# Performance work log

Hardware: AMD Instinct MI355X
Metric: run time of the kernel (lower is better)

Reference implementation:

```python
import jax, jax.numpy as jnp
import numpy as np

B, T, C, H = 4, 2048, 1024, 16
HD = C // H  # head dim = 64


def setup_inputs() -> dict:
    key = jax.random.key(0)
    k1, k2, k3 = jax.random.split(key, 3)
    x = jax.random.normal(k1, (B, T, C), dtype=jnp.float32)
    # nn.Linear weight init scale ~ 1/sqrt(fan_in); keep magnitudes sane
    w_qkv = jax.random.normal(k2, (C, 3 * C), dtype=jnp.float32) * (1.0 / np.sqrt(C))
    w_out = jax.random.normal(k3, (C, C), dtype=jnp.float32) * (1.0 / np.sqrt(C))
    return {"x": x, "w_qkv": w_qkv, "w_out": w_out}


def _attention(x, w_qkv, w_out):
    Bs, Ts, Cs = x.shape
    qkv = x @ w_qkv                                  # [B,T,3C]
    q, k, v = jnp.split(qkv, 3, axis=-1)
    # [B,T,C] -> [B,H,T,hd]
    def heads(t):
        return t.reshape(Bs, Ts, H, HD).transpose(0, 2, 1, 3)
    q, k, v = heads(q), heads(k), heads(v)
    scale = 1.0 / np.sqrt(HD)
    scores = jnp.einsum("bhqd,bhkd->bhqk", q, k) * scale  # [B,H,T,T]
    causal = jnp.tril(jnp.ones((Ts, Ts), dtype=bool))
    scores = jnp.where(causal, scores, jnp.finfo(scores.dtype).min)
    probs = jax.nn.softmax(scores, axis=-1)
    attn = jnp.einsum("bhqk,bhkd->bhqd", probs, v)        # [B,H,T,hd]
    attn = attn.transpose(0, 2, 1, 3).reshape(Bs, Ts, Cs)  # [B,T,C]
    return attn @ w_out  # dropout_p=0 at eval


def reference(x, w_qkv, w_out):
    return _attention(x, w_qkv, w_out)
```

## Files before the change

### kernel.cpp

```cpp
#include <hip/hip_runtime.h>
#include <hip/hip_bf16.h>

#define B_   4
#define T_   2048
#define C_   1024
#define H_   16
#define HD_  64
#define BH_  (B_*H_)
#define M_   (B_*T_)
#define N1_  (3*C_)

typedef __hip_bfloat16 bf16;
typedef __attribute__((ext_vector_type(8))) __bf16 bf16x8v;
typedef __attribute__((ext_vector_type(4))) float  f32x4;

#define QSCALE 0.18033688f

__device__ __forceinline__ f32x4 mfma16(bf16x8v a, bf16x8v b, f32x4 c) {
    return __builtin_amdgcn_mfma_f32_16x16x32_bf16(a, b, c, 0, 0, 0);
}

__device__ __forceinline__ float exp2_hw(float x) {
    return __builtin_amdgcn_exp2f(x);
}

typedef __attribute__((address_space(3))) unsigned int       lds_u32;
typedef const __attribute__((address_space(1))) unsigned int glb_u32;
__device__ __forceinline__ void async16(void* lds, const void* g) {
    __builtin_amdgcn_global_load_lds((glb_u32*)g, (lds_u32*)lds, 16, 0, 0);
}

template<int CTRL>
__device__ __forceinline__ float dpp_rot(float x) {
    int v = __builtin_amdgcn_update_dpp(0, __float_as_int(x), CTRL, 0xF, 0xF, true);
    return __int_as_float(v);
}
__device__ __forceinline__ float row16_sum(float x) {
    x += dpp_rot<0x121>(x);
    x += dpp_rot<0x122>(x);
    x += dpp_rot<0x124>(x);
    x += dpp_rot<0x128>(x);
    return x;
}

__global__ void convert_f32_bf16(const float* __restrict__ in, bf16* __restrict__ out) {
    const int i = blockIdx.x * blockDim.x + threadIdx.x;
    float f[8];
    *(float4*)(f)     = ((const float4*)in)[i*2];
    *(float4*)(f + 4) = ((const float4*)in)[i*2 + 1];
    bf16 t[8];
#pragma unroll
    for (int j = 0; j < 8; ++j) t[j] = __float2bfloat16(f[j]);
    ((uint4*)out)[i] = *(uint4*)t;
}

__global__ void transpose_f32_to_bf16(const float* __restrict__ in,
                                      bf16* __restrict__ out, int K, int N) {
    __shared__ float t[32][33];
    const int n0 = blockIdx.x * 32, k0 = blockIdx.y * 32;
    const int c  = threadIdx.x & 31;
    const int rr = threadIdx.x >> 5;
#pragma unroll
    for (int i = 0; i < 4; ++i)
        t[c][rr + 8*i] = in[(size_t)(k0 + rr + 8*i) * N + n0 + c];
    __syncthreads();
#pragma unroll
    for (int i = 0; i < 4; ++i)
        out[(size_t)(n0 + rr + 8*i) * K + k0 + c] = __float2bfloat16(t[rr + 8*i][c]);
}

template<int EPI>
__global__ __launch_bounds__(256, 2)
void gemm_lds(const bf16* __restrict__ A, const bf16* __restrict__ Bt,
              float* __restrict__ Cmat, int N, int K,
              bf16* __restrict__ qb, bf16* __restrict__ kb, bf16* __restrict__ vb)
{
    __shared__ bf16 Alds[128][32];
    __shared__ bf16 Blds[128][32];

    const int tid  = threadIdx.x;
    const int wave = tid >> 6, lane = tid & 63;
    const int quad = lane >> 4, l16 = lane & 15;
    const int wm   = (wave >> 1) * 64, wn = (wave & 1) * 64;
    const size_t row0 = (size_t)blockIdx.y * 128;
    const size_t col0 = (size_t)blockIdx.x * 128;

    const f32x4 z4 = {0.f, 0.f, 0.f, 0.f};
    f32x4 acc[4][4];
#pragma unroll
    for (int mi = 0; mi < 4; ++mi)
#pragma unroll
        for (int ni = 0; ni < 4; ++ni) acc[mi][ni] = z4;

    const int sr = lane >> 2;
    const int sc = (((lane & 3) ^ ((lane >> 3) & 3))) * 8;
    const bf16* gA0 = A  + (row0 + wave*32 + sr) * (size_t)K + sc;
    const bf16* gA1 = gA0 + (size_t)16 * K;
    const bf16* gB0 = Bt + (col0 + wave*32 + sr) * (size_t)K + sc;
    const bf16* gB1 = gB0 + (size_t)16 * K;
    bf16* lA0 = &Alds[wave*32][0];
    bf16* lA1 = &Alds[wave*32 + 16][0];
    bf16* lB0 = &Blds[wave*32][0];
    bf16* lB1 = &Blds[wave*32 + 16][0];

    const int fg = (quad ^ ((l16 >> 1) & 3)) * 8;

    for (int k0 = 0; k0 < K; k0 += 32) {
        async16(lA0, gA0 + k0);
        async16(lA1, gA1 + k0);
        async16(lB0, gB0 + k0);
        async16(lB1, gB1 + k0);
        __syncthreads();

        bf16x8v af[4], bfr[4];
#pragma unroll
        for (int i = 0; i < 4; ++i) {
            af[i]  = *(const bf16x8v*)(&Alds[wm + i*16 + l16][fg]);
            bfr[i] = *(const bf16x8v*)(&Blds[wn + i*16 + l16][fg]);
        }
#pragma unroll
        for (int mi = 0; mi < 4; ++mi)
#pragma unroll
            for (int ni = 0; ni < 4; ++ni)
                acc[mi][ni] = mfma16(af[mi], bfr[ni], acc[mi][ni]);
        __syncthreads();
    }

#pragma unroll
    for (int mi = 0; mi < 4; ++mi) {
        const size_t rowb = row0 + wm + mi*16 + quad*4;
#pragma unroll
        for (int ni = 0; ni < 4; ++ni) {
            const size_t col = col0 + wn + ni*16 + l16;
#pragma unroll
            for (int r = 0; r < 4; ++r) {
                const float v = acc[mi][ni][r];
                if constexpr (EPI == 0) {
                    Cmat[(rowb + r) * N + col] = v;
                } else {
                    const int rowi = (int)(rowb + r);
                    const int b  = rowi >> 11;
                    const int t  = rowi & (T_ - 1);
                    const int coli = (int)col;
                    const int type = coli >> 10;
                    const int cc2  = coli & (C_ - 1);
                    const int h = cc2 >> 6, d = cc2 & (HD_ - 1);
                    const int bh = b * H_ + h;
                    if (type == 0)
                        qb[((size_t)bh * T_ + t) * HD_ + d] = __float2bfloat16(v * QSCALE);
                    else if (type == 1)
                        kb[((size_t)bh * T_ + t) * HD_ + d] = __float2bfloat16(v);
                    else
                        vb[((size_t)bh * HD_ + d) * T_ + t] = __float2bfloat16(v);
                }
            }
        }
    }
}

#define KP 72
#define VP 72
#define PP 72

__global__ __launch_bounds__(256, 2)
void attn_pair(const bf16* __restrict__ qb, const bf16* __restrict__ kb,
               const bf16* __restrict__ vb, bf16* __restrict__ attn)
{
    __shared__ bf16 Klds[2][64][KP];
    __shared__ bf16 Vlds[2][64][VP];
    __shared__ bf16 Plds[4][32][PP];

    const int tid  = threadIdx.x;
    const int wave = tid >> 6, lane = tid & 63;
    const int quad = lane >> 4, l16 = lane & 15;
    const int bh   = blockIdx.y;

    const bf16* Q  = qb + (size_t)bh * T_ * HD_;
    const bf16* Kp = kb + (size_t)bh * T_ * HD_;
    const bf16* Vp = vb + (size_t)bh * HD_ * T_;

    const int kr = tid >> 3;
    const int kc = (tid & 7) * 8;

    const int b = bh >> 4, h = bh & (H_ - 1);
    const f32x4 z4 = {0.f, 0.f, 0.f, 0.f};

    const int tiles[2] = { (int)blockIdx.x, 15 - (int)blockIdx.x };

    uint4 kreg0 = *(const uint4*)(Kp + (size_t)kr        * HD_ + kc);
    uint4 kreg1 = *(const uint4*)(Kp + (size_t)(kr + 32) * HD_ + kc);
    uint4 vreg0 = *(const uint4*)(Vp + (size_t)kr        * T_  + kc);
    uint4 vreg1 = *(const uint4*)(Vp + (size_t)(kr + 32) * T_  + kc);

    int p = 0;

#pragma unroll 1
    for (int tt = 0; tt < 2; ++tt) {
        const int q0b = tiles[tt] * 128;
        const int q0w = q0b + wave * 32;

        bf16x8v qf[2][2];
#pragma unroll
        for (int mi = 0; mi < 2; ++mi)
#pragma unroll
            for (int kp = 0; kp < 2; ++kp)
                qf[mi][kp] = *(const bf16x8v*)(Q + (size_t)(q0w + mi*16 + l16) * HD_ + kp*32 + quad*8);

        f32x4 o[2][4];
#pragma unroll
        for (int mi = 0; mi < 2; ++mi)
#pragma unroll
            for (int di = 0; di < 4; ++di) o[mi][di] = z4;
        float l_r[2][4];
#pragma unroll
        for (int mi = 0; mi < 2; ++mi)
#pragma unroll
            for (int r = 0; r < 4; ++r) l_r[mi][r] = 0.f;

        const int kend = q0b + 128;

#pragma unroll 1
        for (int k0 = 0; k0 < kend; k0 += 64) {
            *(uint4*)(&Klds[p][kr][kc])      = kreg0;
            *(uint4*)(&Klds[p][kr + 32][kc]) = kreg1;
            *(uint4*)(&Vlds[p][kr][kc])      = vreg0;
            *(uint4*)(&Vlds[p][kr + 32][kc]) = vreg1;
            __syncthreads();

            const int kn = (k0 + 64 < kend) ? (k0 + 64) : 0;
            kreg0 = *(const uint4*)(Kp + (size_t)(kn + kr)      * HD_ + kc);
            kreg1 = *(const uint4*)(Kp + (size_t)(kn + kr + 32) * HD_ + kc);
            vreg0 = *(const uint4*)(Vp + (size_t)kr        * T_ + kn + kc);
            vreg1 = *(const uint4*)(Vp + (size_t)(kr + 32) * T_ + kn + kc);

            if (k0 <= q0w + 31) {
                f32x4 s[2][4];
#pragma unroll
                for (int mi = 0; mi < 2; ++mi)
#pragma unroll
                    for (int ni = 0; ni < 4; ++ni) s[mi][ni] = z4;
#pragma unroll
                for (int kp = 0; kp < 2; ++kp) {
#pragma unroll
                    for (int ni = 0; ni < 4; ++ni) {
                        const bf16x8v kf = *(const bf16x8v*)(&Klds[p][ni*16 + l16][kp*32 + quad*8]);
                        s[0][ni] = mfma16(qf[0][kp], kf, s[0][ni]);
                        s[1][ni] = mfma16(qf[1][kp], kf, s[1][ni]);
                    }
                }
                if (k0 + 63 > q0w) {
#pragma unroll
                    for (int mi = 0; mi < 2; ++mi)
#pragma unroll
                        for (int r = 0; r < 4; ++r) {
                            const int row = q0w + mi*16 + quad*4 + r;
#pragma unroll
                            for (int ni = 0; ni < 4; ++ni)
                                if (k0 + ni*16 + l16 > row) s[mi][ni][r] = -3.0e38f;
                        }
                }
#pragma unroll
                for (int mi = 0; mi < 2; ++mi) {
#pragma unroll
                    for (int r = 0; r < 4; ++r) {
                        float e[4];
#pragma unroll
                        for (int ni = 0; ni < 4; ++ni) e[ni] = exp2_hw(s[mi][ni][r]);
                        l_r[mi][r] += (e[0] + e[1]) + (e[2] + e[3]);
                        const int prow = mi*16 + quad*4 + r;
#pragma unroll
                        for (int ni = 0; ni < 4; ++ni)
                            Plds[wave][prow][ni*16 + l16] = __float2bfloat16(e[ni]);
                    }
                }
                bf16x8v pa[2][2];
#pragma unroll
                for (int mi = 0; mi < 2; ++mi)
#pragma unroll
                    for (int kp = 0; kp < 2; ++kp)
                        pa[mi][kp] = *(const bf16x8v*)(&Plds[wave][mi*16 + l16][kp*32 + quad*8]);
#pragma unroll
                for (int kp = 0; kp < 2; ++kp)
#pragma unroll
                    for (int di = 0; di < 4; ++di) {
                        const bf16x8v vf = *(const bf16x8v*)(&Vlds[p][di*16 + l16][kp*32 + quad*8]);
                        o[0][di] = mfma16(pa[0][kp], vf, o[0][di]);
                        o[1][di] = mfma16(pa[1][kp], vf, o[1][di]);
                    }
            }
            p ^= 1;
        }

#pragma unroll
        for (int mi = 0; mi < 2; ++mi) {
#pragma unroll
            for (int r = 0; r < 4; ++r) {
                const float inv = 1.0f / row16_sum(l_r[mi][r]);
                const int t = q0w + mi*16 + quad*4 + r;
                const size_t base = ((size_t)(b * T_ + t)) * C_ + h * HD_;
#pragma unroll
                for (int di = 0; di < 4; ++di)
                    attn[base + di*16 + l16] = __float2bfloat16(o[mi][di][r] * inv);
            }
        }
    }
}

extern "C" void kernel_launch(void* const* d_in, const int* in_sizes, int n_in,
                              void* d_out, int out_size, void* d_ws, size_t ws_size,
                              hipStream_t stream)
{
    const float* x     = (const float*)d_in[0];
    const float* w_qkv = (const float*)d_in[1];
    const float* w_out = (const float*)d_in[2];
    float* out = (float*)d_out;

    char* ws = (char*)d_ws;
    bf16* qb     = (bf16*)(ws);
    bf16* kb     = (bf16*)(ws + (size_t)16 * 1024 * 1024);
    bf16* vb     = (bf16*)(ws + (size_t)32 * 1024 * 1024);
    bf16* xb     = (bf16*)(ws + (size_t)48 * 1024 * 1024);
    bf16* attnb  = xb;
    bf16* wtqkv  = (bf16*)(ws + (size_t)64 * 1024 * 1024);
    bf16* wtout  = (bf16*)(ws + (size_t)70 * 1024 * 1024);

    convert_f32_bf16<<<dim3((M_*C_)/(8*256)), 256, 0, stream>>>(x, xb);

    transpose_f32_to_bf16<<<dim3(N1_/32, C_/32), 256, 0, stream>>>(w_qkv, wtqkv, C_, N1_);
    transpose_f32_to_bf16<<<dim3(C_/32,  C_/32), 256, 0, stream>>>(w_out, wtout, C_, C_);

    gemm_lds<1><<<dim3(N1_/128, M_/128), 256, 0, stream>>>(
        xb, wtqkv, nullptr, N1_, C_, qb, kb, vb);

    attn_pair<<<dim3(8, BH_), 256, 0, stream>>>(qb, kb, vb, attnb);

    gemm_lds<0><<<dim3(C_/128, M_/128), 256, 0, stream>>>(
        attnb, wtout, out, C_, C_, nullptr, nullptr, nullptr);
}
```

Before: 265.7 us.

## Compute transposed scores to keep P in registers; widen GEMM K-tile

```diff
diff --git a/kernel.cpp b/kernel.cpp
--- a/kernel.cpp
+++ b/kernel.cpp
@@ -30,19 +30,6 @@
     __builtin_amdgcn_global_load_lds((glb_u32*)g, (lds_u32*)lds, 16, 0, 0);
 }
 
-template<int CTRL>
-__device__ __forceinline__ float dpp_rot(float x) {
-    int v = __builtin_amdgcn_update_dpp(0, __float_as_int(x), CTRL, 0xF, 0xF, true);
-    return __int_as_float(v);
-}
-__device__ __forceinline__ float row16_sum(float x) {
-    x += dpp_rot<0x121>(x);
-    x += dpp_rot<0x122>(x);
-    x += dpp_rot<0x124>(x);
-    x += dpp_rot<0x128>(x);
-    return x;
-}
-
 __global__ void convert_f32_bf16(const float* __restrict__ in, bf16* __restrict__ out) {
     const int i = blockIdx.x * blockDim.x + threadIdx.x;
     float f[8];
@@ -75,8 +62,8 @@
               float* __restrict__ Cmat, int N, int K,
               bf16* __restrict__ qb, bf16* __restrict__ kb, bf16* __restrict__ vb)
 {
-    __shared__ bf16 Alds[128][32];
-    __shared__ bf16 Blds[128][32];
+    __shared__ bf16 Alds[128][64];
+    __shared__ bf16 Blds[128][64];
 
     const int tid  = threadIdx.x;
     const int wave = tid >> 6, lane = tid & 63;
@@ -92,37 +79,39 @@
 #pragma unroll
         for (int ni = 0; ni < 4; ++ni) acc[mi][ni] = z4;
 
-    const int sr = lane >> 2;
-    const int sc = (((lane & 3) ^ ((lane >> 3) & 3))) * 8;
-    const bf16* gA0 = A  + (row0 + wave*32 + sr) * (size_t)K + sc;
-    const bf16* gA1 = gA0 + (size_t)16 * K;
-    const bf16* gB0 = Bt + (col0 + wave*32 + sr) * (size_t)K + sc;
-    const bf16* gB1 = gB0 + (size_t)16 * K;
-    bf16* lA0 = &Alds[wave*32][0];
-    bf16* lA1 = &Alds[wave*32 + 16][0];
-    bf16* lB0 = &Blds[wave*32][0];
-    bf16* lB1 = &Blds[wave*32 + 16][0];
-
-    const int fg = (quad ^ ((l16 >> 1) & 3)) * 8;
-
-    for (int k0 = 0; k0 < K; k0 += 32) {
-        async16(lA0, gA0 + k0);
-        async16(lA1, gA1 + k0);
-        async16(lB0, gB0 + k0);
-        async16(lB1, gB1 + k0);
+    const int grow = lane >> 3;
+    const int gcol = ((lane & 7) ^ (lane >> 3)) * 8;
+    const bf16* pA = A  + (row0 + wave*32 + grow) * (size_t)K + gcol;
+    const bf16* pB = Bt + (col0 + wave*32 + grow) * (size_t)K + gcol;
+    bf16* lA = &Alds[wave*32][0];
+    bf16* lB = &Blds[wave*32][0];
+
+    const int fsw = (l16 & 7);
+
+    for (int k0 = 0; k0 < K; k0 += 64) {
+#pragma unroll
+        for (int j = 0; j < 4; ++j)
+            async16(lA + j*512, pA + (size_t)j*8*K + k0);
+#pragma unroll
+        for (int j = 0; j < 4; ++j)
+            async16(lB + j*512, pB + (size_t)j*8*K + k0);
         __syncthreads();
 
-        bf16x8v af[4], bfr[4];
-#pragma unroll
-        for (int i = 0; i < 4; ++i) {
-            af[i]  = *(const bf16x8v*)(&Alds[wm + i*16 + l16][fg]);
-            bfr[i] = *(const bf16x8v*)(&Blds[wn + i*16 + l16][fg]);
-        }
-#pragma unroll
-        for (int mi = 0; mi < 4; ++mi)
-#pragma unroll
-            for (int ni = 0; ni < 4; ++ni)
-                acc[mi][ni] = mfma16(af[mi], bfr[ni], acc[mi][ni]);
+#pragma unroll
+        for (int kp = 0; kp < 2; ++kp) {
+            const int fg = ((kp*4 + quad) ^ fsw) * 8;
+            bf16x8v af[4], bfr[4];
+#pragma unroll
+            for (int i = 0; i < 4; ++i) {
+                af[i]  = *(const bf16x8v*)(&Alds[wm + i*16 + l16][fg]);
+                bfr[i] = *(const bf16x8v*)(&Blds[wn + i*16 + l16][fg]);
+            }
+#pragma unroll
+            for (int mi = 0; mi < 4; ++mi)
+#pragma unroll
+                for (int ni = 0; ni < 4; ++ni)
+                    acc[mi][ni] = mfma16(af[mi], bfr[ni], acc[mi][ni]);
+        }
         __syncthreads();
     }
 
@@ -160,15 +149,14 @@
 
 #define KP 72
 #define VP 72
-#define PP 72
-
-__global__ __launch_bounds__(256, 2)
+
+__global__ __launch_bounds__(256, 3)
 void attn_pair(const bf16* __restrict__ qb, const bf16* __restrict__ kb,
                const bf16* __restrict__ vb, bf16* __restrict__ attn)
 {
     __shared__ bf16 Klds[2][64][KP];
     __shared__ bf16 Vlds[2][64][VP];
-    __shared__ bf16 Plds[4][32][PP];
+    __shared__ float Llds[4][2][16];
 
     const int tid  = threadIdx.x;
     const int wave = tid >> 6, lane = tid & 63;
@@ -185,6 +173,8 @@
     const int b = bh >> 4, h = bh & (H_ - 1);
     const f32x4 z4 = {0.f, 0.f, 0.f, 0.f};
 
+    const int krow_base = ((l16 >> 2) * 8) + (l16 & 3);
+
     const int tiles[2] = { (int)blockIdx.x, 15 - (int)blockIdx.x };
 
     uint4 kreg0 = *(const uint4*)(Kp + (size_t)kr        * HD_ + kc);
@@ -201,21 +191,17 @@
 
         bf16x8v qf[2][2];
 #pragma unroll
-        for (int mi = 0; mi < 2; ++mi)
+        for (int nq = 0; nq < 2; ++nq)
 #pragma unroll
             for (int kp = 0; kp < 2; ++kp)
-                qf[mi][kp] = *(const bf16x8v*)(Q + (size_t)(q0w + mi*16 + l16) * HD_ + kp*32 + quad*8);
+                qf[nq][kp] = *(const bf16x8v*)(Q + (size_t)(q0w + nq*16 + l16) * HD_ + kp*32 + quad*8);
 
         f32x4 o[2][4];
 #pragma unroll
-        for (int mi = 0; mi < 2; ++mi)
-#pragma unroll
-            for (int di = 0; di < 4; ++di) o[mi][di] = z4;
-        float l_r[2][4];
-#pragma unroll
-        for (int mi = 0; mi < 2; ++mi)
-#pragma unroll
-            for (int r = 0; r < 4; ++r) l_r[mi][r] = 0.f;
+        for (int nq = 0; nq < 2; ++nq)
+#pragma unroll
+            for (int di = 0; di < 4; ++di) o[nq][di] = z4;
+        float l_nq[2] = {0.f, 0.f};
 
         const int kend = q0b + 128;
 
@@ -234,51 +220,57 @@
             vreg1 = *(const uint4*)(Vp + (size_t)(kr + 32) * T_ + kn + kc);
 
             if (k0 <= q0w + 31) {
-                f32x4 s[2][4];
-#pragma unroll
-                for (int mi = 0; mi < 2; ++mi)
-#pragma unroll
-                    for (int ni = 0; ni < 4; ++ni) s[mi][ni] = z4;
+                f32x4 st[4][2];
+#pragma unroll
+                for (int mk = 0; mk < 4; ++mk)
+#pragma unroll
+                    for (int nq = 0; nq < 2; ++nq) st[mk][nq] = z4;
 #pragma unroll
                 for (int kp = 0; kp < 2; ++kp) {
-#pragma unroll
-                    for (int ni = 0; ni < 4; ++ni) {
-                        const bf16x8v kf = *(const bf16x8v*)(&Klds[p][ni*16 + l16][kp*32 + quad*8]);
-                        s[0][ni] = mfma16(qf[0][kp], kf, s[0][ni]);
-                        s[1][ni] = mfma16(qf[1][kp], kf, s[1][ni]);
+                    bf16x8v kf[4];
+#pragma unroll
+                    for (int mk = 0; mk < 4; ++mk)
+                        kf[mk] = *(const bf16x8v*)(&Klds[p][krow_base + (mk>>1)*32 + (mk&1)*4][kp*32 + quad*8]);
+#pragma unroll
+                    for (int mk = 0; mk < 4; ++mk) {
+                        st[mk][0] = mfma16(kf[mk], qf[0][kp], st[mk][0]);
+                        st[mk][1] = mfma16(kf[mk], qf[1][kp], st[mk][1]);
                     }
                 }
                 if (k0 + 63 > q0w) {
 #pragma unroll
-                    for (int mi = 0; mi < 2; ++mi)
-#pragma unroll
-                        for (int r = 0; r < 4; ++r) {
-                            const int row = q0w + mi*16 + quad*4 + r;
-#pragma unroll
-                            for (int ni = 0; ni < 4; ++ni)
-                                if (k0 + ni*16 + l16 > row) s[mi][ni][r] = -3.0e38f;
+                    for (int mk = 0; mk < 4; ++mk) {
+                        const int keyb = k0 + (mk>>1)*32 + quad*8 + (mk&1)*4;
+#pragma unroll
+                        for (int nq = 0; nq < 2; ++nq) {
+                            const int qrow = q0w + nq*16 + l16;
+#pragma unroll
+                            for (int r = 0; r < 4; ++r)
+                                if (keyb + r > qrow) st[mk][nq][r] = -3.0e38f;
                         }
-                }
-#pragma unroll
-                for (int mi = 0; mi < 2; ++mi) {
-#pragma unroll
-                    for (int r = 0; r < 4; ++r) {
-                        float e[4];
-#pragma unroll
-                        for (int ni = 0; ni < 4; ++ni) e[ni] = exp2_hw(s[mi][ni][r]);
-                        l_r[mi][r] += (e[0] + e[1]) + (e[2] + e[3]);
-                        const int prow = mi*16 + quad*4 + r;
-#pragma unroll
-                        for (int ni = 0; ni < 4; ++ni)
-                            Plds[wave][prow][ni*16 + l16] = __float2bfloat16(e[ni]);
                     }
                 }
                 bf16x8v pa[2][2];
 #pragma unroll
-                for (int mi = 0; mi < 2; ++mi)
-#pragma unroll
-                    for (int kp = 0; kp < 2; ++kp)
-                        pa[mi][kp] = *(const bf16x8v*)(&Plds[wave][mi*16 + l16][kp*32 + quad*8]);
+                for (int nq = 0; nq < 2; ++nq) {
+#pragma unroll
+                    for (int kp = 0; kp < 2; ++kp) {
+                        union { bf16x8v v; bf16 hh[8]; } u;
+                        float sum = 0.f;
+#pragma unroll
+                        for (int jh = 0; jh < 2; ++jh) {
+                            const int mk = kp*2 + jh;
+#pragma unroll
+                            for (int r = 0; r < 4; ++r) {
+                                const float e = exp2_hw(st[mk][nq][r]);
+                                sum += e;
+                                u.hh[jh*4 + r] = __float2bfloat16(e);
+                            }
+                        }
+                        l_nq[nq] += sum;
+                        pa[nq][kp] = u.v;
+                    }
+                }
 #pragma unroll
                 for (int kp = 0; kp < 2; ++kp)
 #pragma unroll
@@ -292,15 +284,23 @@
         }
 
 #pragma unroll
-        for (int mi = 0; mi < 2; ++mi) {
+        for (int nq = 0; nq < 2; ++nq) {
+            float l = l_nq[nq];
+            l += __shfl_xor(l, 16);
+            l += __shfl_xor(l, 32);
+            if (quad == 0) Llds[wave][nq][l16] = l;
+        }
+#pragma unroll
+        for (int nq = 0; nq < 2; ++nq) {
+            const f32x4 lv = *(const f32x4*)(&Llds[wave][nq][quad*4]);
 #pragma unroll
             for (int r = 0; r < 4; ++r) {
-                const float inv = 1.0f / row16_sum(l_r[mi][r]);
-                const int t = q0w + mi*16 + quad*4 + r;
+                const float inv = 1.0f / lv[r];
+                const int t = q0w + nq*16 + quad*4 + r;
                 const size_t base = ((size_t)(b * T_ + t)) * C_ + h * HD_;
 #pragma unroll
                 for (int di = 0; di < 4; ++di)
-                    attn[base + di*16 + l16] = __float2bfloat16(o[mi][di][r] * inv);
+                    attn[base + di*16 + l16] = __float2bfloat16(o[nq][di][r] * inv);
             }
         }
     }
```

Result: faster. 251.1 us (-5.5%).
